# Optimization experiments

Hardware: AMD Instinct MI355X
Metric: run time of the kernel (lower is better)

Reference implementation:

```python
import jax, jax.numpy as jnp
import numpy as np

N_NODES = 100000
N_EDGES = 1_600_000
D_IN = 128
D_OUT = 128


def setup_inputs() -> dict:
    key = jax.random.key(0)
    k1, k2, k3 = jax.random.split(key, 3)
    input_matrix = jax.random.normal(k1, (N_NODES, D_IN), dtype=jnp.float32)
    adjacency_coo_matrix = jax.random.randint(k2, (2, N_EDGES), 0, N_NODES, dtype=jnp.int64)
    # xavier-uniform-style init for the weight matrix
    limit = float(np.sqrt(6.0 / (D_IN + D_OUT)))
    weights_matrix = jax.random.uniform(k3, (D_IN, D_OUT), dtype=jnp.float32, minval=-limit, maxval=limit)
    return {
        "input_matrix": input_matrix,
        "adjacency_coo_matrix": adjacency_coo_matrix,
        "weights_matrix": weights_matrix,
    }


def reference(input_matrix, adjacency_coo_matrix, weights_matrix):
    # Edge-wise gathers (the irregular-access pattern from the torch code)
    src_idx = adjacency_coo_matrix[0]
    dst_idx = adjacency_coo_matrix[1]
    neighbors = input_matrix[dst_idx]  # [E, D_IN] gather of neighbor features
    # Mean-aggregate neighbor features onto each src node
    agg = jax.ops.segment_sum(neighbors, src_idx, num_segments=N_NODES)  # [N, D_IN]
    deg = jax.ops.segment_sum(jnp.ones((neighbors.shape[0],), dtype=input_matrix.dtype),
                              src_idx, num_segments=N_NODES)  # [N]
    mean_agg = agg / jnp.maximum(deg, 1.0)[:, None]
    # Linear transform with the layer weight matrix
    out = mean_agg @ weights_matrix  # [N, D_OUT]
    return out
```

## Files before the change

kernel.cpp:

```cpp
#include <hip/hip_runtime.h>

#define NN 100000
#define NE 1600000
#define DD 128
#define CAP 64
#define SLICE_N 12500
#define FILL_BLOCKS 2048
#define BPS (FILL_BLOCKS / 8)
#define NGRP (NE / 4)
#define GEMM_BLOCKS ((NN + 63) / 64)
#define LDSP 136

typedef __bf16 bf16x8 __attribute__((ext_vector_type(8)));
typedef float  f32x4  __attribute__((ext_vector_type(4)));
typedef unsigned int u32x4 __attribute__((ext_vector_type(4)));

__device__ __forceinline__ unsigned int f2bf(float f) {
    unsigned int u = __float_as_uint(f);
    return (u + 0x7FFFu + ((u >> 16) & 1u)) >> 16;
}
__device__ __forceinline__ float bflo(unsigned int u) { return __uint_as_float(u << 16); }
__device__ __forceinline__ float bfhi(unsigned int u) { return __uint_as_float(u & 0xFFFF0000u); }

__global__ __launch_bounds__(256) void k_prep(const float* __restrict__ W,
                                              unsigned short* __restrict__ wtb,
                                              int* __restrict__ cnt)
{
    const int idx = blockIdx.x * 256 + (int)threadIdx.x;
    const int k = idx >> 7, n = idx & 127;
    wtb[n * DD + k] = (unsigned short)f2bf(W[idx]);
    int4* c4 = (int4*)cnt;
    for (int i = idx; i < NN / 4; i += DD * DD) c4[i] = make_int4(0, 0, 0, 0);
}

__global__ __launch_bounds__(256, 8) void k_fused(const int* __restrict__ adj,
                                                  int* __restrict__ cnt,
                                                  int* __restrict__ edge_dst,
                                                  const float* __restrict__ x,
                                                  const unsigned short* __restrict__ wtb,
                                                  unsigned short* __restrict__ y)
{
    __shared__ unsigned short ytile[64 * LDSP];

    const int b   = (int)blockIdx.x;
    const int tid = (int)threadIdx.x;

    {
        const int slice = b & 7;
        const int w     = b >> 3;
        const int lo    = slice * SLICE_N;
        const u32x4* src4 = (const u32x4*)adj;
        const u32x4* dst4 = (const u32x4*)(adj + NE);
        const int stride  = BPS * 256;

        for (int g = w * 256 + tid; g < NGRP; g += stride) {
            const u32x4 s4 = __builtin_nontemporal_load(src4 + g);
            const u32x4 d4 = __builtin_nontemporal_load(dst4 + g);
            int sv[4], dv[4], slot[4];
            #pragma unroll
            for (int j = 0; j < 4; ++j) { sv[j] = (int)s4[j]; dv[j] = (int)d4[j]; }
            #pragma unroll
            for (int j = 0; j < 4; ++j) {
                slot[j] = ((unsigned)(sv[j] - lo) < (unsigned)SLICE_N)
                          ? atomicAdd(&cnt[sv[j]], 1) : CAP;
            }
            #pragma unroll
            for (int j = 0; j < 4; ++j) {
                if (slot[j] < CAP)
                    __builtin_nontemporal_store(dv[j],
                        edge_dst + (size_t)sv[j] * CAP + slot[j]);
            }
        }
    }

    if (b >= GEMM_BLOCKS) return;

    const int wave = tid >> 6;
    const int lane = tid & 63;
    const int quad = lane >> 4;
    const int l16  = lane & 15;
    const int mbase = b * 64 + wave * 16;
    const int m = mbase + l16;

    bf16x8 a[4];
    if (m < NN) {
        const float* arow = x + (size_t)m * DD + quad * 8;
        #pragma unroll
        for (int ks = 0; ks < 4; ++ks) {
            const f32x4 f0 = __builtin_nontemporal_load((const f32x4*)(arow + ks * 32));
            const f32x4 f1 = __builtin_nontemporal_load((const f32x4*)(arow + ks * 32 + 4));
            u32x4 p;
            p[0] = f2bf(f0[0]) | (f2bf(f0[1]) << 16);
            p[1] = f2bf(f0[2]) | (f2bf(f0[3]) << 16);
            p[2] = f2bf(f1[0]) | (f2bf(f1[1]) << 16);
            p[3] = f2bf(f1[2]) | (f2bf(f1[3]) << 16);
            a[ks] = __builtin_bit_cast(bf16x8, p);
        }
    } else {
        const u32x4 z = 0;
        #pragma unroll
        for (int ks = 0; ks < 4; ++ks) a[ks] = __builtin_bit_cast(bf16x8, z);
    }

    unsigned short* lrow = ytile + wave * 16 * LDSP;

    #pragma unroll
    for (int nt = 0; nt < 8; ++nt) {
        f32x4 c = {0.f, 0.f, 0.f, 0.f};
        const unsigned short* bcol = wtb + (nt * 16 + l16) * DD + quad * 8;
        #pragma unroll
        for (int ks = 0; ks < 4; ++ks) {
            const bf16x8 bb = __builtin_bit_cast(bf16x8, *(const uint4*)(bcol + ks * 32));
            c = __builtin_amdgcn_mfma_f32_16x16x32_bf16(a[ks], bb, c, 0, 0, 0);
        }
        #pragma unroll
        for (int r = 0; r < 4; ++r)
            lrow[(quad * 4 + r) * LDSP + nt * 16 + l16] = (unsigned short)f2bf(c[r]);
    }

    __syncthreads();

    const int r16   = lane >> 2;
    const int ch    = lane & 3;
    const int growr = b * 64 + wave * 16 + r16;
    if (growr < NN) {
        const unsigned short* lsrc = ytile + (wave * 16 + r16) * LDSP + ch * 32;
        unsigned short* gdst = y + (size_t)growr * DD + ch * 32;
        *(uint4*)(gdst + 0)  = *(const uint4*)(lsrc + 0);
        *(uint4*)(gdst + 8)  = *(const uint4*)(lsrc + 8);
        *(uint4*)(gdst + 16) = *(const uint4*)(lsrc + 16);
        *(uint4*)(gdst + 24) = *(const uint4*)(lsrc + 24);
    }
}

__global__ __launch_bounds__(256) void k_agg3(const unsigned short* __restrict__ y,
                                              const int* __restrict__ cnt,
                                              const int* __restrict__ edge_dst,
                                              float* __restrict__ out)
{
    const int tid  = (int)threadIdx.x;
    const int wave = tid >> 6;
    const int lane = tid & 63;
    const int eg   = lane >> 4;
    const int h    = lane & 15;
    const int n    = (int)blockIdx.x * 16 + wave * 4 + eg;

    int deg = cnt[n];
    if (deg > CAP) deg = CAP;
    const int* el = edge_dst + (size_t)n * CAP;

    float acc[8] = {0.f,0.f,0.f,0.f,0.f,0.f,0.f,0.f};

    #define ACC(p) do {                                         \
        acc[0] += bflo((p).x); acc[1] += bfhi((p).x);           \
        acc[2] += bflo((p).y); acc[3] += bfhi((p).y);           \
        acc[4] += bflo((p).z); acc[5] += bfhi((p).z);           \
        acc[6] += bflo((p).w); acc[7] += bfhi((p).w);           \
    } while (0)

    int i = 0;
    for (; i + 7 < deg; i += 8) {
        const int d0 = el[i];
        const int d1 = el[i + 1];
        const int d2 = el[i + 2];
        const int d3 = el[i + 3];
        const int d4 = el[i + 4];
        const int d5 = el[i + 5];
        const int d6 = el[i + 6];
        const int d7 = el[i + 7];
        const uint4 p0 = *(const uint4*)(y + (size_t)d0 * DD + h * 8);
        const uint4 p1 = *(const uint4*)(y + (size_t)d1 * DD + h * 8);
        const uint4 p2 = *(const uint4*)(y + (size_t)d2 * DD + h * 8);
        const uint4 p3 = *(const uint4*)(y + (size_t)d3 * DD + h * 8);
        const uint4 p4 = *(const uint4*)(y + (size_t)d4 * DD + h * 8);
        const uint4 p5 = *(const uint4*)(y + (size_t)d5 * DD + h * 8);
        const uint4 p6 = *(const uint4*)(y + (size_t)d6 * DD + h * 8);
        const uint4 p7 = *(const uint4*)(y + (size_t)d7 * DD + h * 8);
        ACC(p0); ACC(p1); ACC(p2); ACC(p3);
        ACC(p4); ACC(p5); ACC(p6); ACC(p7);
    }
    for (; i + 3 < deg; i += 4) {
        const int d0 = el[i];
        const int d1 = el[i + 1];
        const int d2 = el[i + 2];
        const int d3 = el[i + 3];
        const uint4 p0 = *(const uint4*)(y + (size_t)d0 * DD + h * 8);
        const uint4 p1 = *(const uint4*)(y + (size_t)d1 * DD + h * 8);
        const uint4 p2 = *(const uint4*)(y + (size_t)d2 * DD + h * 8);
        const uint4 p3 = *(const uint4*)(y + (size_t)d3 * DD + h * 8);
        ACC(p0); ACC(p1); ACC(p2); ACC(p3);
    }
    for (; i < deg; ++i) {
        const int d0 = el[i];
        const uint4 p0 = *(const uint4*)(y + (size_t)d0 * DD + h * 8);
        ACC(p0);
    }
    #undef ACC

    const float inv = 1.0f / fmaxf((float)deg, 1.0f);
    float* o = out + (size_t)n * DD + h * 8;
    float4 w0 = {acc[0]*inv, acc[1]*inv, acc[2]*inv, acc[3]*inv};
    float4 w1 = {acc[4]*inv, acc[5]*inv, acc[6]*inv, acc[7]*inv};
    *(float4*)(o + 0) = w0;
    *(float4*)(o + 4) = w1;
}

extern "C" void kernel_launch(void* const* d_in, const int* in_sizes, int n_in,
                              void* d_out, int out_size, void* d_ws, size_t ws_size,
                              hipStream_t stream) {
    const float* x   = (const float*)d_in[0];
    const int*   adj = (const int*)d_in[1];
    const float* W   = (const float*)d_in[2];
    float* out = (float*)d_out;

    unsigned short* y   = (unsigned short*)d_ws;
    unsigned short* wtb = y + (size_t)NN * DD;
    int* cnt      = (int*)(wtb + DD * DD);
    int* edge_dst = cnt + NN;

    k_prep <<<DD * DD / 256, 256, 0, stream>>>(W, wtb, cnt);
    k_fused<<<FILL_BLOCKS, 256, 0, stream>>>(adj, cnt, edge_dst, x, wtb, y);
    k_agg3 <<<NN / 16, 256, 0, stream>>>(y, cnt, edge_dst, out);
}
```

Before: 266.6 us.

## Split node aggregation across a whole wave and prefetch GEMM inputs early

The aggregation kernel now gives each node a full 64-lane wave. Four edge groups stride through the neighbour list, and their partial sums are combined with cross-lane shuffles, replacing one 16-lane group per node. This exposes more independent gathers per node to hide latency for high-degree nodes, at the cost of four times as many blocks, shuffle reductions, and idle lanes on the final store. The fused kernel also issues its x-row loads before the edge-bucketing loop so their latency overlaps the atomics. The edge list stores switch from nontemporal to normal stores. Holding 32 extra float registers across the fill loop could reduce occupancy.

```diff
diff --git a/kernel.cpp b/kernel.cpp
--- a/kernel.cpp
+++ b/kernel.cpp
@@ -44,6 +44,23 @@
 
     const int b   = (int)blockIdx.x;
     const int tid = (int)threadIdx.x;
+    const int wave = tid >> 6;
+    const int lane = tid & 63;
+    const int quad = lane >> 4;
+    const int l16  = lane & 15;
+    const int mbase = b * 64 + wave * 16;
+    const int m = mbase + l16;
+
+    f32x4 af[8];
+    const bool amask = (b < GEMM_BLOCKS) && (m < NN);
+    if (amask) {
+        const float* arow = x + (size_t)m * DD + quad * 8;
+        #pragma unroll
+        for (int ks = 0; ks < 4; ++ks) {
+            af[2 * ks + 0] = __builtin_nontemporal_load((const f32x4*)(arow + ks * 32));
+            af[2 * ks + 1] = __builtin_nontemporal_load((const f32x4*)(arow + ks * 32 + 4));
+        }
+    }
 
     {
         const int slice = b & 7;
@@ -67,28 +84,19 @@
             #pragma unroll
             for (int j = 0; j < 4; ++j) {
                 if (slot[j] < CAP)
-                    __builtin_nontemporal_store(dv[j],
-                        edge_dst + (size_t)sv[j] * CAP + slot[j]);
+                    edge_dst[(size_t)sv[j] * CAP + slot[j]] = dv[j];
             }
         }
     }
 
     if (b >= GEMM_BLOCKS) return;
 
-    const int wave = tid >> 6;
-    const int lane = tid & 63;
-    const int quad = lane >> 4;
-    const int l16  = lane & 15;
-    const int mbase = b * 64 + wave * 16;
-    const int m = mbase + l16;
-
     bf16x8 a[4];
-    if (m < NN) {
-        const float* arow = x + (size_t)m * DD + quad * 8;
+    if (amask) {
         #pragma unroll
         for (int ks = 0; ks < 4; ++ks) {
-            const f32x4 f0 = __builtin_nontemporal_load((const f32x4*)(arow + ks * 32));
-            const f32x4 f1 = __builtin_nontemporal_load((const f32x4*)(arow + ks * 32 + 4));
+            const f32x4 f0 = af[2 * ks + 0];
+            const f32x4 f1 = af[2 * ks + 1];
             u32x4 p;
             p[0] = f2bf(f0[0]) | (f2bf(f0[1]) << 16);
             p[1] = f2bf(f0[2]) | (f2bf(f0[3]) << 16);
@@ -133,18 +141,15 @@
     }
 }
 
-__global__ __launch_bounds__(256) void k_agg3(const unsigned short* __restrict__ y,
+__global__ __launch_bounds__(256) void k_agg2(const unsigned short* __restrict__ y,
                                               const int* __restrict__ cnt,
                                               const int* __restrict__ edge_dst,
                                               float* __restrict__ out)
 {
-    const int tid  = (int)threadIdx.x;
-    const int wave = tid >> 6;
-    const int lane = tid & 63;
+    const int n    = blockIdx.x * 4 + ((int)threadIdx.x >> 6);
+    const int lane = (int)threadIdx.x & 63;
     const int eg   = lane >> 4;
     const int h    = lane & 15;
-    const int n    = (int)blockIdx.x * 16 + wave * 4 + eg;
-
     int deg = cnt[n];
     if (deg > CAP) deg = CAP;
     const int* el = edge_dst + (size_t)n * CAP;
@@ -158,51 +163,46 @@
         acc[6] += bflo((p).w); acc[7] += bfhi((p).w);           \
     } while (0)
 
-    int i = 0;
-    for (; i + 7 < deg; i += 8) {
+    int i = eg;
+    for (; i + 12 < deg; i += 16) {
         const int d0 = el[i];
-        const int d1 = el[i + 1];
-        const int d2 = el[i + 2];
-        const int d3 = el[i + 3];
-        const int d4 = el[i + 4];
-        const int d5 = el[i + 5];
-        const int d6 = el[i + 6];
-        const int d7 = el[i + 7];
-        const uint4 p0 = *(const uint4*)(y + (size_t)d0 * DD + h * 8);
-        const uint4 p1 = *(const uint4*)(y + (size_t)d1 * DD + h * 8);
-        const uint4 p2 = *(const uint4*)(y + (size_t)d2 * DD + h * 8);
-        const uint4 p3 = *(const uint4*)(y + (size_t)d3 * DD + h * 8);
-        const uint4 p4 = *(const uint4*)(y + (size_t)d4 * DD + h * 8);
-        const uint4 p5 = *(const uint4*)(y + (size_t)d5 * DD + h * 8);
-        const uint4 p6 = *(const uint4*)(y + (size_t)d6 * DD + h * 8);
-        const uint4 p7 = *(const uint4*)(y + (size_t)d7 * DD + h * 8);
-        ACC(p0); ACC(p1); ACC(p2); ACC(p3);
-        ACC(p4); ACC(p5); ACC(p6); ACC(p7);
-    }
-    for (; i + 3 < deg; i += 4) {
-        const int d0 = el[i];
-        const int d1 = el[i + 1];
-        const int d2 = el[i + 2];
-        const int d3 = el[i + 3];
+        const int d1 = el[i + 4];
+        const int d2 = el[i + 8];
+        const int d3 = el[i + 12];
         const uint4 p0 = *(const uint4*)(y + (size_t)d0 * DD + h * 8);
         const uint4 p1 = *(const uint4*)(y + (size_t)d1 * DD + h * 8);
         const uint4 p2 = *(const uint4*)(y + (size_t)d2 * DD + h * 8);
         const uint4 p3 = *(const uint4*)(y + (size_t)d3 * DD + h * 8);
         ACC(p0); ACC(p1); ACC(p2); ACC(p3);
     }
-    for (; i < deg; ++i) {
+    for (; i + 4 < deg; i += 8) {
+        const int d0 = el[i];
+        const int d1 = el[i + 4];
+        const uint4 p0 = *(const uint4*)(y + (size_t)d0 * DD + h * 8);
+        const uint4 p1 = *(const uint4*)(y + (size_t)d1 * DD + h * 8);
+        ACC(p0); ACC(p1);
+    }
+    for (; i < deg; i += 4) {
         const int d0 = el[i];
         const uint4 p0 = *(const uint4*)(y + (size_t)d0 * DD + h * 8);
         ACC(p0);
     }
     #undef ACC
 
-    const float inv = 1.0f / fmaxf((float)deg, 1.0f);
-    float* o = out + (size_t)n * DD + h * 8;
-    float4 w0 = {acc[0]*inv, acc[1]*inv, acc[2]*inv, acc[3]*inv};
-    float4 w1 = {acc[4]*inv, acc[5]*inv, acc[6]*inv, acc[7]*inv};
-    *(float4*)(o + 0) = w0;
-    *(float4*)(o + 4) = w1;
+    #pragma unroll
+    for (int j = 0; j < 8; ++j) {
+        acc[j] += __shfl_xor(acc[j], 16, 64);
+        acc[j] += __shfl_xor(acc[j], 32, 64);
+    }
+
+    if (eg == 0) {
+        const float inv = 1.0f / fmaxf((float)deg, 1.0f);
+        float* o = out + (size_t)n * DD + h * 8;
+        float4 w0 = {acc[0]*inv, acc[1]*inv, acc[2]*inv, acc[3]*inv};
+        float4 w1 = {acc[4]*inv, acc[5]*inv, acc[6]*inv, acc[7]*inv};
+        *(float4*)(o + 0) = w0;
+        *(float4*)(o + 4) = w1;
+    }
 }
 
 extern "C" void kernel_launch(void* const* d_in, const int* in_sizes, int n_in,
@@ -220,5 +220,5 @@
 
     k_prep <<<DD * DD / 256, 256, 0, stream>>>(W, wtb, cnt);
     k_fused<<<FILL_BLOCKS, 256, 0, stream>>>(adj, cnt, edge_dst, x, wtb, y);
-    k_agg3 <<<NN / 16, 256, 0, stream>>>(y, cnt, edge_dst, out);
-}
+    k_agg2 <<<NN / 4, 256, 0, stream>>>(y, cnt, edge_dst, out);
+}
```

New measurement: 254.3 us. 1.05x faster.
